# Kernel optimization log

Measured on AMD Instinct MI355X. Metric: run time of the kernel, lower is better.

Reference implementation:

```python
import jax, jax.numpy as jnp
import numpy as np

IN_F, HID, N_CLS = 128, 256, 2
N_NODES, N_EDGES = 50000, 800000


def setup_inputs() -> dict:
    key = jax.random.key(0)
    ks = jax.random.split(key, 8)
    x = jax.random.normal(ks[0], (N_NODES, IN_F), dtype=jnp.float32)
    edge_index = jax.random.randint(ks[1], (2, N_EDGES), 0, N_NODES, dtype=jnp.int64)
    # Linear params (torch nn.Linear: y = x @ W.T + b), uniform(-1/sqrt(fan_in), ..)
    def lin(k, out_f, in_f):
        k1, k2 = jax.random.split(k)
        bound = 1.0 / np.sqrt(in_f)
        W = jax.random.uniform(k1, (out_f, in_f), minval=-bound, maxval=bound, dtype=jnp.float32)
        b = jax.random.uniform(k2, (out_f,), minval=-bound, maxval=bound, dtype=jnp.float32)
        return W, b
    W1, b1 = lin(ks[2], HID, IN_F)
    W2, b2 = lin(ks[3], HID // 2, HID)
    W3, b3 = lin(ks[4], N_CLS, HID // 2)
    return {"x": x, "edge_index": edge_index, "n_nodes": N_NODES,
            "W1": W1, "b1": b1, "W2": W2, "b2": b2, "W3": W3, "b3": b3}


def _gcn_layer(x, row, col, deg_inv, n_nodes, W, b):
    # gather neighbor features, scatter-add into destinations, degree-normalize
    agg = jax.ops.segment_sum(x[row], col, num_segments=n_nodes)  # [N, F]
    agg = agg * deg_inv[:, None]
    return agg @ W.T + b


def reference(x, edge_index, n_nodes, W1, b1, W2, b2, W3, b3):
    row, col = edge_index[0], edge_index[1]
    deg = jax.ops.segment_sum(jnp.ones_like(col, dtype=x.dtype), col, num_segments=n_nodes)
    deg_inv = 1.0 / jnp.maximum(deg, 1.0)  # bincount().clamp(min=1)
    h = jax.nn.relu(_gcn_layer(x, row, col, deg_inv, n_nodes, W1, b1))
    # dropout is identity in eval mode
    h = jax.nn.relu(_gcn_layer(h, row, col, deg_inv, n_nodes, W2, b2))
    return h @ W3.T + b3  # [N, num_classes]
```

## Files before the change

kernel.cpp:

```cpp
#include <hip/hip_runtime.h>
#include <hip/hip_fp16.h>

#define IN_F 128
#define HID 256
#define HID2 128
#define MAXDEG 64
#define NPART 8

typedef __attribute__((ext_vector_type(8))) _Float16 f16x8;
typedef __attribute__((ext_vector_type(4))) float f32x4;

__global__ __launch_bounds__(256) void prep(
        const float* __restrict__ x,
        const float* __restrict__ W1, const float* __restrict__ W2,
        ushort* __restrict__ xh, ushort* __restrict__ w1p, ushort* __restrict__ w2p,
        int* __restrict__ fill, int N) {
    int gid = blockIdx.x * 256 + threadIdx.x, gsz = gridDim.x * 256;
    for (int i = gid; i < N; i += gsz) fill[i] = 0;
    int t8 = N * IN_F / 8;
    for (int i = gid; i < t8; i += gsz) {
        const float4* s4 = (const float4*)x + (size_t)i * 2;
        float4 f0 = s4[0], f1 = s4[1];
        uint4 o;
        o.x = __half_as_ushort(__float2half(f0.x)) | ((unsigned)__half_as_ushort(__float2half(f0.y)) << 16);
        o.y = __half_as_ushort(__float2half(f0.z)) | ((unsigned)__half_as_ushort(__float2half(f0.w)) << 16);
        o.z = __half_as_ushort(__float2half(f1.x)) | ((unsigned)__half_as_ushort(__float2half(f1.y)) << 16);
        o.w = __half_as_ushort(__float2half(f1.z)) | ((unsigned)__half_as_ushort(__float2half(f1.w)) << 16);
        ((uint4*)xh)[i] = o;
    }
    for (int i = gid; i < 65536; i += gsz) {
        int l = (i >> 3) & 63, plane = (i >> 9) & 1, j = (i >> 10) & 1;
        int k4 = (i >> 11) & 3, wvv = (i >> 13) & 7;
        int q = l >> 4, rr = l & 15;
        int n = wvv * 32 + 16 * j + rr;
        int k = k4 * 32 + q * 8 + (i & 7);
        float f = W1[n * IN_F + k];
        __half hh = __float2half(f);
        w1p[i] = plane ? __half_as_ushort(__float2half(f - __half2float(hh)))
                       : __half_as_ushort(hh);
    }
    for (int i = gid; i < 65536; i += gsz) {
        int l = (i >> 3) & 63, plane = (i >> 9) & 1, j = (i >> 10) & 1;
        int kk = (i >> 11) & 7, g = (i >> 14) & 3;
        int q = l >> 4, rr = l & 15;
        int n = g * 32 + 16 * j + rr;
        int k = kk * 32 + q * 8 + (i & 7);
        float f = W2[n * HID + k];
        __half hh = __float2half(f);
        w2p[i] = plane ? __half_as_ushort(__float2half(f - __half2float(hh)))
                       : __half_as_ushort(hh);
    }
}

__global__ __launch_bounds__(256) void fill_csr(const int* __restrict__ row,
                                                const int* __restrict__ col,
                                                int* __restrict__ fill,
                                                ushort* __restrict__ csr,
                                                int E, int npp) {
    int part = blockIdx.x & (NPART - 1);
    int bi   = blockIdx.x >> 3;
    int bpp  = gridDim.x >> 3;
    int lo = part * npp, hi = lo + npp;
    for (int e = bi * 256 + threadIdx.x; e < E; e += bpp * 256) {
        int c = col[e];
        if (c >= lo && c < hi) {
            int p = atomicAdd(&fill[c], 1);
            if (p < MAXDEG) csr[(size_t)c * MAXDEG + p] = (ushort)row[e];
        }
    }
}

__device__ __forceinline__ void add8h(float4& lo, float4& hi, uint4 v) {
    float2 f0 = __half22float2(*(const __half2*)&v.x);
    float2 f1 = __half22float2(*(const __half2*)&v.y);
    float2 f2 = __half22float2(*(const __half2*)&v.z);
    float2 f3 = __half22float2(*(const __half2*)&v.w);
    lo.x += f0.x; lo.y += f0.y; lo.z += f1.x; lo.w += f1.y;
    hi.x += f2.x; hi.y += f2.y; hi.z += f3.x; hi.w += f3.y;
}

__global__ __launch_bounds__(256, 8) void agg_gather(const ushort* __restrict__ xh,
                                                  const int* __restrict__ deg,
                                                  const ushort* __restrict__ csr,
                                                  ushort* __restrict__ outh, int N) {
    int w = threadIdx.x >> 6, lane = threadIdx.x & 63;
    int n = blockIdx.x * 4 + w;
    if (n >= N) return;
    int d = deg[n]; if (d > MAXDEG) d = MAXDEG;
    int s = n * MAXDEG;
    int q = lane >> 4, l16 = lane & 15;
    int myidx = (int)csr[s + lane];
    const uint4* xv = (const uint4*)xh;
    float4 L0={0,0,0,0},H0={0,0,0,0},L1={0,0,0,0},H1={0,0,0,0};
    float4 L2={0,0,0,0},H2={0,0,0,0},L3={0,0,0,0},H3={0,0,0,0};
    int i = 0;
    for (; i + 15 < d; i += 16) {
        int e0 = __shfl(myidx, i + q, 64);
        int e1 = __shfl(myidx, i + 4 + q, 64);
        int e2 = __shfl(myidx, i + 8 + q, 64);
        int e3 = __shfl(myidx, i + 12 + q, 64);
        uint4 v0 = xv[(size_t)e0 * 16 + l16];
        uint4 v1 = xv[(size_t)e1 * 16 + l16];
        uint4 v2 = xv[(size_t)e2 * 16 + l16];
        uint4 v3 = xv[(size_t)e3 * 16 + l16];
        add8h(L0, H0, v0); add8h(L1, H1, v1); add8h(L2, H2, v2); add8h(L3, H3, v3);
    }
    for (; i + 3 < d; i += 4) {
        int e0 = __shfl(myidx, i + q, 64);
        add8h(L0, H0, xv[(size_t)e0 * 16 + l16]);
    }
    {
        int rem = d - i;
        int e0 = __shfl(myidx, (i + q) & 63, 64);
        if (q < rem) add8h(L0, H0, xv[(size_t)e0 * 16 + l16]);
    }
    L0.x+=L1.x+L2.x+L3.x; L0.y+=L1.y+L2.y+L3.y; L0.z+=L1.z+L2.z+L3.z; L0.w+=L1.w+L2.w+L3.w;
    H0.x+=H1.x+H2.x+H3.x; H0.y+=H1.y+H2.y+H3.y; H0.z+=H1.z+H2.z+H3.z; H0.w+=H1.w+H2.w+H3.w;
#define XRED(v) v += __shfl_xor(v, 16, 64); v += __shfl_xor(v, 32, 64)
    XRED(L0.x); XRED(L0.y); XRED(L0.z); XRED(L0.w);
    XRED(H0.x); XRED(H0.y); XRED(H0.z); XRED(H0.w);
    if (q == 0) {
        float dinv = 1.f / fmaxf((float)d, 1.f);
        uint4 o;
        o.x = __half_as_ushort(__float2half(L0.x * dinv)) |
              ((unsigned)__half_as_ushort(__float2half(L0.y * dinv)) << 16);
        o.y = __half_as_ushort(__float2half(L0.z * dinv)) |
              ((unsigned)__half_as_ushort(__float2half(L0.w * dinv)) << 16);
        o.z = __half_as_ushort(__float2half(H0.x * dinv)) |
              ((unsigned)__half_as_ushort(__float2half(H0.y * dinv)) << 16);
        o.w = __half_as_ushort(__float2half(H0.z * dinv)) |
              ((unsigned)__half_as_ushort(__float2half(H0.w * dinv)) << 16);
        ((uint4*)outh)[(size_t)n * 16 + l16] = o;
    }
}

__global__ __launch_bounds__(512, 1) void gemm_fused(const ushort* __restrict__ A,
                                                     const ushort* __restrict__ w1p,
                                                     const ushort* __restrict__ w2p,
                                                     const float* __restrict__ b1,
                                                     ushort* __restrict__ Z,
                                                     int M, int nt) {
    __shared__ uint4 AbufV[2048];
    __shared__ uint4 hsbV[2048];
    char* hsb  = (char*)hsbV;
    int t = threadIdx.x;
    int wv = t >> 6, l = t & 63, r = l & 15, q = l >> 4;

    const int arow0 = t >> 4, seg0 = t & 15;
    const int dst0 = arow0 * 256 + ((seg0 ^ (arow0 & 7)) << 4);

    uint4 pv0, pv1;
    {
        int m0 = blockIdx.x * 64;
        int ma = m0 + arow0;      if (ma > M - 1) ma = M - 1;
        int mb = m0 + arow0 + 32; if (mb > M - 1) mb = M - 1;
        pv0 = *(const uint4*)((const char*)A + (size_t)ma * 256 + seg0 * 16);
        pv1 = *(const uint4*)((const char*)A + (size_t)mb * 256 + seg0 * 16);
    }

    f16x8 w1f[4][2][2];
#pragma unroll
    for (int k4 = 0; k4 < 4; k4++)
#pragma unroll
        for (int j = 0; j < 2; j++)
#pragma unroll
            for (int p = 0; p < 2; p++)
                w1f[k4][j][p] = *(const f16x8*)((const _Float16*)w1p +
                                  ((((wv * 4 + k4) * 2 + j) * 2 + p) * 512 + l * 8));
    int g = wv & 3;
    f16x8 w2f[8][2][2];
#pragma unroll
    for (int kk = 0; kk < 8; kk++)
#pragma unroll
        for (int j = 0; j < 2; j++)
#pragma unroll
            for (int p = 0; p < 2; p++)
                w2f[kk][j][p] = *(const f16x8*)((const _Float16*)w2p +
                                  ((((g * 8 + kk) * 2 + j) * 2 + p) * 512 + l * 8));

    int nA0 = wv * 32;
    float bo0 = b1[nA0 + r], bo1 = b1[nA0 + 16 + r];
    int mbB = (wv >> 2) * 32, nB0 = (wv & 3) * 32;

    int cur = 0;
    for (int tile = blockIdx.x; tile < nt; tile += gridDim.x) {
        int m0 = tile * 64;
        char* Abuf = (char*)(AbufV + cur * 1024);
        *(uint4*)(Abuf + dst0)        = pv0;
        *(uint4*)(Abuf + dst0 + 8192) = pv1;
        __syncthreads();
        int nxt = tile + gridDim.x;
        if (nxt < nt) {
            int m0n = nxt * 64;
            int ma = m0n + arow0;      if (ma > M - 1) ma = M - 1;
            int mb2 = m0n + arow0 + 32; if (mb2 > M - 1) mb2 = M - 1;
            pv0 = *(const uint4*)((const char*)A + (size_t)ma * 256 + seg0 * 16);
            pv1 = *(const uint4*)((const char*)A + (size_t)mb2 * 256 + seg0 * 16);
        }

        f32x4 acc[4][2];
#pragma unroll
        for (int i = 0; i < 4; i++)
#pragma unroll
            for (int j = 0; j < 2; j++) acc[i][j] = (f32x4){0.f, 0.f, 0.f, 0.f};
#pragma unroll
        for (int k4 = 0; k4 < 4; k4++) {
            f16x8 a[4];
#pragma unroll
            for (int i = 0; i < 4; i++) {
                int arow = 16 * i + r;
                a[i] = *(const f16x8*)(Abuf + arow * 256 + (((k4 * 4 + q) ^ (arow & 7)) << 4));
            }
#pragma unroll
            for (int i = 0; i < 4; i++)
#pragma unroll
                for (int j = 0; j < 2; j++) {
                    acc[i][j] = __builtin_amdgcn_mfma_f32_16x16x32_f16(a[i], w1f[k4][j][0], acc[i][j], 0, 0, 0);
                    acc[i][j] = __builtin_amdgcn_mfma_f32_16x16x32_f16(a[i], w1f[k4][j][1], acc[i][j], 0, 0, 0);
                }
        }
#pragma unroll
        for (int j = 0; j < 2; j++) {
            float bo = j ? bo1 : bo0;
            int n = nA0 + 16 * j + r;
#pragma unroll
            for (int i = 0; i < 4; i++)
#pragma unroll
                for (int reg = 0; reg < 4; reg++) {
                    int mr = 16 * i + q * 4 + reg;
                    *(_Float16*)(hsb + mr * 512 + ((((n >> 3) ^ (mr & 7)) << 4)) + (n & 7) * 2)
                        = (_Float16)fmaxf(acc[i][j][reg] + bo, 0.f);
                }
        }
        __syncthreads();

        f32x4 accB[2][2];
#pragma unroll
        for (int i = 0; i < 2; i++)
#pragma unroll
            for (int j = 0; j < 2; j++) accB[i][j] = (f32x4){0.f, 0.f, 0.f, 0.f};
#pragma unroll
        for (int kk = 0; kk < 8; kk++) {
            f16x8 a[2];
#pragma unroll
            for (int i = 0; i < 2; i++) {
                int hrow = mbB + 16 * i + r;
                a[i] = *(const f16x8*)(hsb + hrow * 512 + (((kk * 4 + q) ^ (hrow & 7)) << 4));
            }
#pragma unroll
            for (int i = 0; i < 2; i++)
#pragma unroll
                for (int j = 0; j < 2; j++) {
                    accB[i][j] = __builtin_amdgcn_mfma_f32_16x16x32_f16(a[i], w2f[kk][j][0], accB[i][j], 0, 0, 0);
                    accB[i][j] = __builtin_amdgcn_mfma_f32_16x16x32_f16(a[i], w2f[kk][j][1], accB[i][j], 0, 0, 0);
                }
        }
#pragma unroll
        for (int i = 0; i < 2; i++)
#pragma unroll
            for (int reg = 0; reg < 4; reg++) {
                int m = m0 + mbB + 16 * i + q * 4 + reg;
                if (m < M) {
#pragma unroll
                    for (int j = 0; j < 2; j++) {
                        int n = nB0 + 16 * j + r;
                        Z[(size_t)m * HID2 + n] = __half_as_ushort(__float2half(accB[i][j][reg]));
                    }
                }
            }
        cur ^= 1;
    }
}

__global__ __launch_bounds__(256, 8) void agg2_out(const ushort* __restrict__ zh,
                                                const int* __restrict__ deg,
                                                const ushort* __restrict__ csr,
                                                const float* __restrict__ b2,
                                                const float* __restrict__ W3,
                                                const float* __restrict__ b3,
                                                float* __restrict__ out, int N) {
    int w = threadIdx.x >> 6, lane = threadIdx.x & 63;
    int n = blockIdx.x * 4 + w;
    if (n >= N) return;
    int d = deg[n]; if (d > MAXDEG) d = MAXDEG;
    int s = n * MAXDEG;
    int q = lane >> 4, l16 = lane & 15;
    int myidx = (int)csr[s + lane];
    const uint4* zv = (const uint4*)zh;
    float4 L0={0,0,0,0},H0={0,0,0,0},L1={0,0,0,0},H1={0,0,0,0};
    float4 L2={0,0,0,0},H2={0,0,0,0},L3={0,0,0,0},H3={0,0,0,0};
    int i = 0;
    for (; i + 15 < d; i += 16) {
        int e0 = __shfl(myidx, i + q, 64);
        int e1 = __shfl(myidx, i + 4 + q, 64);
        int e2 = __shfl(myidx, i + 8 + q, 64);
        int e3 = __shfl(myidx, i + 12 + q, 64);
        uint4 v0 = zv[(size_t)e0 * 16 + l16];
        uint4 v1 = zv[(size_t)e1 * 16 + l16];
        uint4 v2 = zv[(size_t)e2 * 16 + l16];
        uint4 v3 = zv[(size_t)e3 * 16 + l16];
        add8h(L0, H0, v0); add8h(L1, H1, v1); add8h(L2, H2, v2); add8h(L3, H3, v3);
    }
    for (; i + 3 < d; i += 4) {
        int e0 = __shfl(myidx, i + q, 64);
        add8h(L0, H0, zv[(size_t)e0 * 16 + l16]);
    }
    {
        int rem = d - i;
        int e0 = __shfl(myidx, (i + q) & 63, 64);
        if (q < rem) add8h(L0, H0, zv[(size_t)e0 * 16 + l16]);
    }
    L0.x+=L1.x+L2.x+L3.x; L0.y+=L1.y+L2.y+L3.y; L0.z+=L1.z+L2.z+L3.z; L0.w+=L1.w+L2.w+L3.w;
    H0.x+=H1.x+H2.x+H3.x; H0.y+=H1.y+H2.y+H3.y; H0.z+=H1.z+H2.z+H3.z; H0.w+=H1.w+H2.w+H3.w;
    XRED(L0.x); XRED(L0.y); XRED(L0.z); XRED(L0.w);
    XRED(H0.x); XRED(H0.y); XRED(H0.z); XRED(H0.w);
    float dinv = 1.f / fmaxf((float)d, 1.f);
    float4 b2a = ((const float4*)b2)[l16 * 2],      b2b = ((const float4*)b2)[l16 * 2 + 1];
    float4 w0a = ((const float4*)W3)[l16 * 2],      w0b = ((const float4*)W3)[l16 * 2 + 1];
    float4 w1a = ((const float4*)W3)[32 + l16 * 2], w1b = ((const float4*)W3)[33 + l16 * 2];
    float p0 = 0.f, p1 = 0.f, h;
    h = fmaxf(L0.x * dinv + b2a.x, 0.f); p0 += h * w0a.x; p1 += h * w1a.x;
    h = fmaxf(L0.y * dinv + b2a.y, 0.f); p0 += h * w0a.y; p1 += h * w1a.y;
    h = fmaxf(L0.z * dinv + b2a.z, 0.f); p0 += h * w0a.z; p1 += h * w1a.z;
    h = fmaxf(L0.w * dinv + b2a.w, 0.f); p0 += h * w0a.w; p1 += h * w1a.w;
    h = fmaxf(H0.x * dinv + b2b.x, 0.f); p0 += h * w0b.x; p1 += h * w1b.x;
    h = fmaxf(H0.y * dinv + b2b.y, 0.f); p0 += h * w0b.y; p1 += h * w1b.y;
    h = fmaxf(H0.z * dinv + b2b.z, 0.f); p0 += h * w0b.z; p1 += h * w1b.z;
    h = fmaxf(H0.w * dinv + b2b.w, 0.f); p0 += h * w0b.w; p1 += h * w1b.w;
#pragma unroll
    for (int m2 = 1; m2 <= 32; m2 <<= 1) {
        p0 += __shfl_xor(p0, m2, 64);
        p1 += __shfl_xor(p1, m2, 64);
    }
    if (lane == 0) {
        out[(size_t)n * 2 + 0] = p0 * 0.25f + b3[0];
        out[(size_t)n * 2 + 1] = p1 * 0.25f + b3[1];
    }
}

extern "C" void kernel_launch(void* const* d_in, const int* in_sizes, int n_in,
                              void* d_out, int out_size, void* d_ws, size_t ws_size,
                              hipStream_t stream) {
    const float* x  = (const float*)d_in[0];
    const int*   ei = (const int*)d_in[1];
    const float* W1 = (const float*)d_in[3];
    const float* b1 = (const float*)d_in[4];
    const float* W2 = (const float*)d_in[5];
    const float* b2 = (const float*)d_in[6];
    const float* W3 = (const float*)d_in[7];
    const float* b3 = (const float*)d_in[8];
    float* out = (float*)d_out;

    int N = in_sizes[0] / IN_F;
    int E = in_sizes[1] / 2;
    const int* row = ei;
    const int* col = ei + E;

    char* base = (char*)d_ws;
    size_t off = 0;
    auto alloc = [&](size_t bytes) -> void* {
        off = (off + 255) & ~(size_t)255;
        void* p = base + off;
        off += bytes;
        return p;
    };
    int*    fill = (int*)alloc((size_t)N * 4);
    ushort* csr  = (ushort*)alloc((size_t)N * MAXDEG * 2);
    ushort* xh   = (ushort*)alloc((size_t)N * IN_F * 2);
    ushort* f2h  = (ushort*)alloc((size_t)N * IN_F * 2);
    ushort* z2h  = (ushort*)alloc((size_t)N * HID2 * 2);
    ushort* w1p  = (ushort*)alloc(65536 * 2);
    ushort* w2p  = (ushort*)alloc(65536 * 2);

    int npp = (N + NPART - 1) / NPART;
    int nt = (N + 63) / 64;
    prep<<<2048, 256, 0, stream>>>(x, W1, W2, xh, w1p, w2p, fill, N);
    fill_csr<<<2048, 256, 0, stream>>>(row, col, fill, csr, E, npp);
    agg_gather<<<(N + 3) / 4, 256, 0, stream>>>(xh, fill, csr, f2h, N);
    gemm_fused<<<256, 512, 0, stream>>>(f2h, w1p, w2p, b1, z2h, N, nt);
    agg2_out<<<(N + 3) / 4, 256, 0, stream>>>(z2h, fill, csr, b2, W3, b3, out, N);
}
```

Baseline: 223.4 us.

## Merge fp16 conversion and CSR build into one launch with a separate zero pass

```diff
diff --git a/kernel.cpp b/kernel.cpp
--- a/kernel.cpp
+++ b/kernel.cpp
@@ -6,17 +6,40 @@
 #define HID2 128
 #define MAXDEG 64
 #define NPART 8
+#define PREP_BLOCKS 2048
 
 typedef __attribute__((ext_vector_type(8))) _Float16 f16x8;
 typedef __attribute__((ext_vector_type(4))) float f32x4;
 
-__global__ __launch_bounds__(256) void prep(
+__global__ __launch_bounds__(256) void zero_fill(int* __restrict__ fill, int N) {
+    int gid = blockIdx.x * 256 + threadIdx.x, gsz = gridDim.x * 256;
+    for (int i = gid; i < N; i += gsz) fill[i] = 0;
+}
+
+__global__ __launch_bounds__(256) void prep_fill(
         const float* __restrict__ x,
         const float* __restrict__ W1, const float* __restrict__ W2,
         ushort* __restrict__ xh, ushort* __restrict__ w1p, ushort* __restrict__ w2p,
-        int* __restrict__ fill, int N) {
-    int gid = blockIdx.x * 256 + threadIdx.x, gsz = gridDim.x * 256;
-    for (int i = gid; i < N; i += gsz) fill[i] = 0;
+        const int* __restrict__ row, const int* __restrict__ col,
+        int* __restrict__ fill, ushort* __restrict__ csr,
+        int E, int npp, int N) {
+    int b = blockIdx.x;
+    if (b >= PREP_BLOCKS) {
+        int pb = b - PREP_BLOCKS;
+        int part = pb & (NPART - 1);
+        int bi   = pb >> 3;
+        int bpp  = (gridDim.x - PREP_BLOCKS) >> 3;
+        int lo = part * npp, hi = lo + npp;
+        for (int e = bi * 256 + threadIdx.x; e < E; e += bpp * 256) {
+            int c = col[e];
+            if (c >= lo && c < hi) {
+                int p = atomicAdd(&fill[c], 1);
+                if (p < MAXDEG) csr[(size_t)c * MAXDEG + p] = (ushort)row[e];
+            }
+        }
+        return;
+    }
+    int gid = b * 256 + threadIdx.x, gsz = PREP_BLOCKS * 256;
     int t8 = N * IN_F / 8;
     for (int i = gid; i < t8; i += gsz) {
         const float4* s4 = (const float4*)x + (size_t)i * 2;
@@ -52,24 +75,6 @@
     }
 }
 
-__global__ __launch_bounds__(256) void fill_csr(const int* __restrict__ row,
-                                                const int* __restrict__ col,
-                                                int* __restrict__ fill,
-                                                ushort* __restrict__ csr,
-                                                int E, int npp) {
-    int part = blockIdx.x & (NPART - 1);
-    int bi   = blockIdx.x >> 3;
-    int bpp  = gridDim.x >> 3;
-    int lo = part * npp, hi = lo + npp;
-    for (int e = bi * 256 + threadIdx.x; e < E; e += bpp * 256) {
-        int c = col[e];
-        if (c >= lo && c < hi) {
-            int p = atomicAdd(&fill[c], 1);
-            if (p < MAXDEG) csr[(size_t)c * MAXDEG + p] = (ushort)row[e];
-        }
-    }
-}
-
 __device__ __forceinline__ void add8h(float4& lo, float4& hi, uint4 v) {
     float2 f0 = __half22float2(*(const __half2*)&v.x);
     float2 f1 = __half22float2(*(const __half2*)&v.y);
@@ -78,6 +83,8 @@
     lo.x += f0.x; lo.y += f0.y; lo.z += f1.x; lo.w += f1.y;
     hi.x += f2.x; hi.y += f2.y; hi.z += f3.x; hi.w += f3.y;
 }
+
+#define XRED(v) v += __shfl_xor(v, 16, 64); v += __shfl_xor(v, 32, 64)
 
 __global__ __launch_bounds__(256, 8) void agg_gather(const ushort* __restrict__ xh,
                                                   const int* __restrict__ deg,
@@ -116,7 +123,6 @@
     }
     L0.x+=L1.x+L2.x+L3.x; L0.y+=L1.y+L2.y+L3.y; L0.z+=L1.z+L2.z+L3.z; L0.w+=L1.w+L2.w+L3.w;
     H0.x+=H1.x+H2.x+H3.x; H0.y+=H1.y+H2.y+H3.y; H0.z+=H1.z+H2.z+H3.z; H0.w+=H1.w+H2.w+H3.w;
-#define XRED(v) v += __shfl_xor(v, 16, 64); v += __shfl_xor(v, 32, 64)
     XRED(L0.x); XRED(L0.y); XRED(L0.z); XRED(L0.w);
     XRED(H0.x); XRED(H0.y); XRED(H0.z); XRED(H0.w);
     if (q == 0) {
@@ -192,7 +198,7 @@
         int nxt = tile + gridDim.x;
         if (nxt < nt) {
             int m0n = nxt * 64;
-            int ma = m0n + arow0;      if (ma > M - 1) ma = M - 1;
+            int ma = m0n + arow0;       if (ma > M - 1) ma = M - 1;
             int mb2 = m0n + arow0 + 32; if (mb2 > M - 1) mb2 = M - 1;
             pv0 = *(const uint4*)((const char*)A + (size_t)ma * 256 + seg0 * 16);
             pv1 = *(const uint4*)((const char*)A + (size_t)mb2 * 256 + seg0 * 16);
@@ -374,8 +380,9 @@
 
     int npp = (N + NPART - 1) / NPART;
     int nt = (N + 63) / 64;
-    prep<<<2048, 256, 0, stream>>>(x, W1, W2, xh, w1p, w2p, fill, N);
-    fill_csr<<<2048, 256, 0, stream>>>(row, col, fill, csr, E, npp);
+    zero_fill<<<64, 256, 0, stream>>>(fill, N);
+    prep_fill<<<PREP_BLOCKS + 2048, 256, 0, stream>>>(x, W1, W2, xh, w1p, w2p,
+                                                      row, col, fill, csr, E, npp, N);
     agg_gather<<<(N + 3) / 4, 256, 0, stream>>>(xh, fill, csr, f2h, N);
     gemm_fused<<<256, 512, 0, stream>>>(f2h, w1p, w2p, b1, z2h, N, nt);
     agg2_out<<<(N + 3) / 4, 256, 0, stream>>>(z2h, fill, csr, b2, W3, b3, out, N);
```

Result: no change. 222.3 us (-0.5%).
